# Optimization experiments

Hardware: AMD Instinct MI355X
Metric: run time of the kernel (lower is better)

The kernel has to match this reference:

```python
import jax, jax.numpy as jnp
import numpy as np

B, S, D, H = 2, 2048, 1024, 16
HD = D // H  # head_dim = 64
ROPE_BASE = 10000.0


def _rope_tables(seq_len, head_dim, dtype):
    inv_freq = 1.0 / (ROPE_BASE ** (jnp.arange(0, head_dim, 2, dtype=jnp.float32) / head_dim))
    t = jnp.arange(seq_len, dtype=jnp.float32)
    freqs = jnp.outer(t, inv_freq)                      # [S, HD/2]
    emb = jnp.concatenate([freqs, freqs], axis=-1)      # [S, HD]
    return jnp.cos(emb).astype(dtype), jnp.sin(emb).astype(dtype)


def _rotate_half(x):
    x1, x2 = jnp.split(x, 2, axis=-1)
    return jnp.concatenate([-x2, x1], axis=-1)


def setup_inputs() -> dict:
    key = jax.random.key(0)
    k0, k1, k2, k3, k4 = jax.random.split(key, 5)
    std = 0.02
    return {
        "hidden_states": jax.random.normal(k0, (B, S, D), dtype=jnp.float32),
        "attention_mask": jnp.ones((B, S), dtype=jnp.int32),
        "Wq": jax.random.normal(k1, (D, D), dtype=jnp.float32) * std,
        "Wk": jax.random.normal(k2, (D, D), dtype=jnp.float32) * std,
        "Wv": jax.random.normal(k3, (D, D), dtype=jnp.float32) * std,
        "Wo": jax.random.normal(k4, (D, D), dtype=jnp.float32) * std,
    }


def reference(hidden_states, attention_mask, Wq, Wk, Wv, Wo):
    b, s, d = hidden_states.shape
    scale = HD ** -0.5

    # torch Linear (no bias): y = x @ W.T, then split heads -> [b, h, s, hd]
    def proj_heads(W):
        y = jnp.einsum('bsd,ed->bse', hidden_states, W)
        return y.reshape(b, s, H, HD).transpose(0, 2, 1, 3)

    q, k, v = proj_heads(Wq), proj_heads(Wk), proj_heads(Wv)

    cos, sin = _rope_tables(s, HD, q.dtype)   # [s, hd]
    cos, sin = cos[None, None], sin[None, None]
    q = q * cos + _rotate_half(q) * sin
    k = k * cos + _rotate_half(k) * sin

    attn = jnp.einsum('bhqd,bhkd->bhqk', q, k) * scale  # [b,h,s,s]
    # mask [b,s] broadcast over heads and query dim (matches expand in torch)
    attn = jnp.where(attention_mask[:, None, None, :] == 0, -jnp.inf, attn)
    attn = jax.nn.softmax(attn, axis=-1)

    out = jnp.einsum('bhqk,bhkd->bhqd', attn, v)
    out = out.transpose(0, 2, 1, 3).reshape(b, s, d)
    return jnp.einsum('bsd,ed->bse', out, Wo)
```

## Files before the change

kernel.cpp:

```cpp
#include <hip/hip_runtime.h>
#include <math.h>

#define B_  2
#define S_  2048
#define D_  1024
#define H_  16
#define HD_ 64
#define M_  (B_*S_)

typedef __attribute__((ext_vector_type(8)))  short s8v;
typedef __attribute__((ext_vector_type(4)))  int   i4v;
typedef __attribute__((ext_vector_type(4)))  float f4v;
typedef __attribute__((ext_vector_type(16))) float f16x;
#define MFMA16(a,b,c) __builtin_amdgcn_mfma_f32_16x16x32_bf16(a,b,c,0,0,0)
#define MFMA32(a,b,c) __builtin_amdgcn_mfma_f32_32x32x16_bf16(a,b,c,0,0,0)

typedef __attribute__((address_space(1))) const unsigned int uint_ga;
typedef __attribute__((address_space(3))) unsigned int       uint_ls;

__device__ __forceinline__ unsigned short f2bf(float x) {
    unsigned u = __float_as_uint(x);
    u += 0x7FFF + ((u >> 16) & 1);
    return (unsigned short)(u >> 16);
}
__device__ __forceinline__ void gld16(const unsigned short* g, short* l) {
    __builtin_amdgcn_global_load_lds((uint_ga*)g, (uint_ls*)l, 16, 0, 0);
}

__global__ void rope_table_kernel(float2* __restrict__ cst)
{
    int i = blockIdx.x * 256 + threadIdx.x;
    int j = i >> 11, s = i & 2047;
    double inv = pow(10000.0, -(double)j / 32.0);
    double ang = (double)s * inv;
    cst[i] = make_float2((float)cos(ang), (float)sin(ang));
}

__global__ __launch_bounds__(256) void cvt_bf16_kernel(
    const float* __restrict__ X,  const float* __restrict__ Wq,
    const float* __restrict__ Wk, const float* __restrict__ Wv,
    const float* __restrict__ Wo,
    unsigned short* __restrict__ Xb,  unsigned short* __restrict__ Wqb,
    unsigned short* __restrict__ Wkb, unsigned short* __restrict__ Wvb,
    unsigned short* __restrict__ Wob)
{
    int y = blockIdx.y;
    const float* src = (y==0)?X:(y==1)?Wq:(y==2)?Wk:(y==3)?Wv:Wo;
    unsigned short* dst = (y==0)?Xb:(y==1)?Wqb:(y==2)?Wkb:(y==3)?Wvb:Wob;
    int n = (y==0) ? (M_*D_) : (D_*D_);
    int i = (blockIdx.x*256 + threadIdx.x)*4;
    if (i >= n) return;
    float4 v = *(const float4*)&src[i];
    ushort4 o;
    o.x = f2bf(v.x); o.y = f2bf(v.y); o.z = f2bf(v.z); o.w = f2bf(v.w);
    *(ushort4*)&dst[i] = o;
}

__device__ __forceinline__ void mfma_128x128(
    const unsigned short* __restrict__ Amat, const unsigned short* __restrict__ Bmat,
    int m0, int n0, short* As, short* Bs, f4v acc[4][4])
{
    int tid = threadIdx.x;
    int l = tid & 63, w = tid >> 6;
    int wm = w >> 1, wn = w & 1;
    int lm = l & 15, qd = l >> 4;
    int lm7 = lm & 7;

    f4v z = {0.f, 0.f, 0.f, 0.f};
#pragma unroll
    for (int mt = 0; mt < 4; mt++)
#pragma unroll
        for (int nt = 0; nt < 4; nt++) acc[mt][nt] = z;

    int rl = l >> 3;
    int kc = (l & 7) ^ rl;
    const unsigned short* aG = Amat + (size_t)(m0 + w*32 + rl) * D_ + kc*8;
    const unsigned short* bG = Bmat + (size_t)(n0 + w*32 + rl) * D_ + kc*8;
    short* aL = As + (w*32)*64;
    short* bL = Bs + (w*32)*64;

#pragma unroll 1
    for (int k0 = 0; k0 < D_; k0 += 64) {
        __syncthreads();
#pragma unroll
        for (int j = 0; j < 4; j++) {
            gld16(aG + k0 + (size_t)j*8*D_, aL + j*8*64);
            gld16(bG + k0 + (size_t)j*8*D_, bL + j*8*64);
        }
        __syncthreads();
#pragma unroll
        for (int half = 0; half < 2; half++) {
            int pc = (half*4 + qd) ^ lm7;
            s8v afr[4], bfr[4];
#pragma unroll
            for (int x = 0; x < 4; x++) {
                afr[x] = *(const s8v*)(As + ((wm*64 + x*16 + lm)*8 + pc)*8);
                bfr[x] = *(const s8v*)(Bs + ((wn*64 + x*16 + lm)*8 + pc)*8);
            }
#pragma unroll
            for (int mt = 0; mt < 4; mt++)
#pragma unroll
                for (int nt = 0; nt < 4; nt++)
                    acc[mt][nt] = MFMA16(afr[mt], bfr[nt], acc[mt][nt]);
        }
    }
}

__global__ __launch_bounds__(256, 2) void qkv_mfma_kernel(
    const unsigned short* __restrict__ Xb,
    const unsigned short* __restrict__ Wqb, const unsigned short* __restrict__ Wkb,
    const unsigned short* __restrict__ Wvb, const float2* __restrict__ cst,
    unsigned short* __restrict__ Q, unsigned short* __restrict__ K,
    unsigned short* __restrict__ Vt)
{
    __shared__ __align__(16) short As[8192], Bs[8192];
    int bx = blockIdx.x, by = blockIdx.y;
    int proj = by >> 3, f8 = by & 7;
    int l = threadIdx.x & 63, w = threadIdx.x >> 6;
    int wm = w >> 1, wn = w & 1, lm = l & 15, qd = l >> 4;

    f4v acc[4][4];
    if (proj < 2) {
        const unsigned short* Wm = proj ? Wkb : Wqb;
        mfma_128x128(Wm, Xb, f8*128, bx*128, As, Bs, acc);

        int b  = (bx*128) >> 11;
        int sb = ((bx*128) & 2047) + wn*64;
        int bh = b*H_ + f8*2 + wm;
        unsigned short* dst = proj ? K : Q;
#pragma unroll
        for (int mt = 0; mt < 4; mt++) {
            float sgn = (mt < 2) ? -1.f : 1.f;
#pragma unroll
            for (int nt = 0; nt < 4; nt++) {
                int s = sb + nt*16 + lm;
                unsigned short ov[4];
#pragma unroll
                for (int r = 0; r < 4; r++) {
                    int d = mt*16 + qd*4 + r;
                    float2 cs = cst[(d & 31)*S_ + s];
                    float v = acc[mt][nt][r];
                    float p = acc[mt^2][nt][r];
                    ov[r] = f2bf(v*cs.x + sgn*p*cs.y);
                }
                ushort4 ou; ou.x=ov[0]; ou.y=ov[1]; ou.z=ov[2]; ou.w=ov[3];
                *(ushort4*)&dst[((size_t)bh*S_ + s)*HD_ + mt*16 + qd*4] = ou;
            }
        }
    } else {
        mfma_128x128(Xb, Wvb, bx*128, f8*128, As, Bs, acc);

        int b  = (bx*128) >> 11;
        int sb = ((bx*128) & 2047) + wm*64;
        int bh = b*H_ + f8*2 + wn;
#pragma unroll
        for (int mt = 0; mt < 4; mt++)
#pragma unroll
            for (int nt = 0; nt < 4; nt++) {
                int dim = nt*16 + lm;
                int s   = sb + mt*16 + qd*4;
                ushort4 ou;
                ou.x = f2bf(acc[mt][nt][0]);
                ou.y = f2bf(acc[mt][nt][1]);
                ou.z = f2bf(acc[mt][nt][2]);
                ou.w = f2bf(acc[mt][nt][3]);
                *(ushort4*)&Vt[((size_t)bh*HD_ + dim)*S_ + s] = ou;
            }
    }
}

#define SCALE2 0.1803368801111204f
#define MXF2   16.0f
__global__ __launch_bounds__(256, 2) void flash_mfma_kernel(
    const unsigned short* __restrict__ Q, const unsigned short* __restrict__ K,
    const unsigned short* __restrict__ Vt, const int* __restrict__ mask,
    unsigned short* __restrict__ AO)
{
    __shared__ __align__(16) short Ksh[8192];
    __shared__ __align__(16) short Vsh[8192];
    __shared__ __align__(16) float msk[S_];

    int bh = blockIdx.y;
    int b = bh >> 4, h = bh & 15;
    int tid = threadIdx.x;
    int l = tid & 63, w = tid >> 6;
    int lq = l & 31;
    int hf = l >> 5;
    int q0 = blockIdx.x * 128 + w * 32;

    {
        int i0 = tid * 8;
        const int* mp = mask + b * S_ + i0;
#pragma unroll
        for (int jj = 0; jj < 8; jj++)
            msk[i0 + jj] = mp[jj] ? -MXF2 : -3.0e38f;
    }

    const unsigned short* Qr = Q + ((size_t)bh * S_ + q0 + lq) * HD_ + hf * 8;
    s8v qf[4];
#pragma unroll
    for (int dc = 0; dc < 4; dc++) qf[dc] = *(const s8v*)(Qr + dc * 16);

    f16x zz = {0.f};
    f16x oacc[2]; oacc[0] = zz; oacc[1] = zz;
    float li = 0.f;

    const unsigned short* Kb = K  + (size_t)bh * S_ * HD_;
    const unsigned short* Vb = Vt + (size_t)bh * HD_ * S_;

    int fb0 = 2*w, fb1 = 2*w + 1;
    const unsigned short* kS0 = Kb + (size_t)((fb0>>2)*32 + lq) * HD_ + (fb0&3)*16 + hf*8;
    const unsigned short* kS1 = Kb + (size_t)((fb1>>2)*32 + lq) * HD_ + (fb1&3)*16 + hf*8;
    const unsigned short* vS0 = Vb + (size_t)((fb0>>2)*32 + lq) * S_  + (fb0&3)*16 + hf*8;
    const unsigned short* vS1 = Vb + (size_t)((fb1>>2)*32 + lq) * S_  + (fb1&3)*16 + hf*8;

    s8v kr0 = *(const s8v*)(kS0);
    s8v kr1 = *(const s8v*)(kS1);
    s8v vr0 = *(const s8v*)(vS0);
    s8v vr1 = *(const s8v*)(vS1);

#pragma unroll 1
    for (int t = 0; t < S_ / 64; t++) {
        int buf = (t & 1) * 4096;
        *(s8v*)(Ksh + buf + fb0*512 + l*8) = kr0;
        *(s8v*)(Ksh + buf + fb1*512 + l*8) = kr1;
        *(s8v*)(Vsh + buf + fb0*512 + l*8) = vr0;
        *(s8v*)(Vsh + buf + fb1*512 + l*8) = vr1;
        __syncthreads();
        if (t < S_/64 - 1) {
            int koff = (t + 1) * 64;
            kr0 = *(const s8v*)(kS0 + (size_t)koff * HD_);
            kr1 = *(const s8v*)(kS1 + (size_t)koff * HD_);
            vr0 = *(const s8v*)(vS0 + koff);
            vr1 = *(const s8v*)(vS1 + koff);
        }

        f16x sa0 = zz, sa1 = zz;
#pragma unroll
        for (int dc = 0; dc < 4; dc++) {
            s8v kf0 = *(const s8v*)(Ksh + buf + (0*4 + dc)*512 + l*8);
            sa0 = MFMA32(kf0, qf[dc], sa0);
        }
#pragma unroll
        for (int dc = 0; dc < 4; dc++) {
            s8v kf1 = *(const s8v*)(Ksh + buf + (1*4 + dc)*512 + l*8);
            sa1 = MFMA32(kf1, qf[dc], sa1);
        }

        float p[32];
#pragma unroll
        for (int kt = 0; kt < 2; kt++)
#pragma unroll
            for (int g = 0; g < 4; g++) {
                f4v mv = *(const f4v*)&msk[t*64 + kt*32 + g*8 + hf*4];
#pragma unroll
                for (int i = 0; i < 4; i++) {
                    float raw = (kt == 0) ? sa0[g*4 + i] : sa1[g*4 + i];
                    p[kt*16 + g*4 + i] = exp2f(fmaf(raw, SCALE2, mv[i]));
                }
            }
#pragma unroll
        for (int r = 0; r < 32; r++)
            li += __uint_as_float(__float_as_uint(p[r]) & 0xFFFF0000u);
        int pk[16];
#pragma unroll
        for (int m = 0; m < 16; m++)
            pk[m] = __builtin_amdgcn_perm(__float_as_uint(p[2*m+1]),
                                          __float_as_uint(p[2*m]), 0x07060302);

#pragma unroll
        for (int kc = 0; kc < 4; kc++) {
            int a = 4*kc;
            int x01 = hf ? pk[a]   : pk[a+2];
            int x23 = hf ? pk[a+1] : pk[a+3];
            int y01 = __shfl_xor(x01, 32);
            int y23 = __shfl_xor(x23, 32);
            i4v fr;
            fr.x = hf ? y01 : pk[a];
            fr.y = hf ? y23 : pk[a+1];
            fr.z = hf ? pk[a+2] : y01;
            fr.w = hf ? pk[a+3] : y23;
            s8v pf = __builtin_bit_cast(s8v, fr);
#pragma unroll
            for (int dt = 0; dt < 2; dt++) {
                s8v vf = *(const s8v*)(Vsh + buf + (dt*4 + kc)*512 + l*8);
                oacc[dt] = MFMA32(vf, pf, oacc[dt]);
            }
        }
        __syncthreads();
    }

    li += __shfl_xor(li, 32);
    float invl = 1.0f / li;
    int qtok = q0 + lq;
    unsigned short* Or = AO + ((size_t)(b * S_ + qtok)) * D_ + h * HD_;
#pragma unroll
    for (int dt = 0; dt < 2; dt++)
#pragma unroll
        for (int g = 0; g < 4; g++) {
            int d0 = dt*32 + g*8 + hf*4;
            ushort4 o;
            o.x = f2bf(oacc[dt][g*4 + 0] * invl);
            o.y = f2bf(oacc[dt][g*4 + 1] * invl);
            o.z = f2bf(oacc[dt][g*4 + 2] * invl);
            o.w = f2bf(oacc[dt][g*4 + 3] * invl);
            *(ushort4*)&Or[d0] = o;
        }
}

__global__ __launch_bounds__(256, 2) void outproj_mfma_kernel(
    const unsigned short* __restrict__ AO, const unsigned short* __restrict__ Wob,
    float* __restrict__ out)
{
    __shared__ __align__(16) short As[8192], Bs[8192];
    int bx = blockIdx.x, by = blockIdx.y;
    int l = threadIdx.x & 63, w = threadIdx.x >> 6;
    int wm = w >> 1, wn = w & 1, lm = l & 15, qd = l >> 4;

    f4v acc[4][4];
    mfma_128x128(Wob, AO, by*128, bx*128, As, Bs, acc);

#pragma unroll
    for (int mt = 0; mt < 4; mt++)
#pragma unroll
        for (int nt = 0; nt < 4; nt++) {
            int tok = bx*128 + wn*64 + nt*16 + lm;
            int e   = by*128 + wm*64 + mt*16 + qd*4;
            *(f4v*)&out[(size_t)tok*D_ + e] = acc[mt][nt];
        }
}

extern "C" void kernel_launch(void* const* d_in, const int* in_sizes, int n_in,
                              void* d_out, int out_size, void* d_ws, size_t ws_size,
                              hipStream_t stream)
{
    const float* X    = (const float*)d_in[0];
    const int*   mask = (const int*)  d_in[1];
    const float* Wq   = (const float*)d_in[2];
    const float* Wk   = (const float*)d_in[3];
    const float* Wv   = (const float*)d_in[4];
    const float* Wo   = (const float*)d_in[5];
    float* out = (float*)d_out;

    unsigned short* ws = (unsigned short*)d_ws;
    unsigned short* Xb  = ws;
    unsigned short* Wqb = Xb  + (size_t)M_ * D_;
    unsigned short* Wkb = Wqb + (size_t)D_ * D_;
    unsigned short* Wvb = Wkb + (size_t)D_ * D_;
    unsigned short* Wob = Wvb + (size_t)D_ * D_;
    unsigned short* Qb  = Wob + (size_t)D_ * D_;
    unsigned short* Kb  = Qb  + (size_t)M_ * D_;
    unsigned short* Vtb = Kb  + (size_t)M_ * D_;
    unsigned short* AOb = Vtb + (size_t)M_ * D_;
    float2* cst = (float2*)(AOb + (size_t)M_ * D_);

    rope_table_kernel<<<(S_ * 32) / 256, 256, 0, stream>>>(cst);
    cvt_bf16_kernel<<<dim3(4096, 5), 256, 0, stream>>>(
        X, Wq, Wk, Wv, Wo, Xb, Wqb, Wkb, Wvb, Wob);
    qkv_mfma_kernel<<<dim3(32, 24), 256, 0, stream>>>(
        Xb, Wqb, Wkb, Wvb, cst, Qb, Kb, Vtb);
    flash_mfma_kernel<<<dim3(S_ / 128, B_ * H_), 256, 0, stream>>>(
        Qb, Kb, Vtb, mask, AOb);
    outproj_mfma_kernel<<<dim3(32, 8), 256, 0, stream>>>(AOb, Wob, out);
}
```

Before: 209.4 us.

## Async LDS loads in flash loop, MFMA row sums, fold scale into Q, merge rope kernel

The flash kernel now loads K/V tiles directly into LDS with global_load_lds and double buffers them, which drops the register staging and one barrier per iteration. The softmax denominator is computed by an extra MFMA against a vector of ones instead of 32 scalar adds per lane. The softmax scale is folded into Q during the QKV epilogue, which removes an FMA per score. The rope table computation is merged into the conversion kernel to save one launch. The risks are bf16 rounding of the pre-scaled Q and a possible race, since the next-buffer async load is issued while other waves may still be reading the previous buffer; the trailing barrier appears to protect against this.

```diff
diff --git a/kernel.cpp b/kernel.cpp
--- a/kernel.cpp
+++ b/kernel.cpp
@@ -27,14 +27,8 @@
     __builtin_amdgcn_global_load_lds((uint_ga*)g, (uint_ls*)l, 16, 0, 0);
 }
 
-__global__ void rope_table_kernel(float2* __restrict__ cst)
-{
-    int i = blockIdx.x * 256 + threadIdx.x;
-    int j = i >> 11, s = i & 2047;
-    double inv = pow(10000.0, -(double)j / 32.0);
-    double ang = (double)s * inv;
-    cst[i] = make_float2((float)cos(ang), (float)sin(ang));
-}
+#define SCALE2 0.1803368801111204f
+#define MXF2   16.0f
 
 __global__ __launch_bounds__(256) void cvt_bf16_kernel(
     const float* __restrict__ X,  const float* __restrict__ Wq,
@@ -42,9 +36,19 @@
     const float* __restrict__ Wo,
     unsigned short* __restrict__ Xb,  unsigned short* __restrict__ Wqb,
     unsigned short* __restrict__ Wkb, unsigned short* __restrict__ Wvb,
-    unsigned short* __restrict__ Wob)
+    unsigned short* __restrict__ Wob, float2* __restrict__ cst)
 {
     int y = blockIdx.y;
+    if (y == 5) {
+        int i = blockIdx.x * 256 + threadIdx.x;
+        if (i < S_ * 32) {
+            int j = i >> 11, s = i & 2047;
+            double inv = pow(10000.0, -(double)j / 32.0);
+            double ang = (double)s * inv;
+            cst[i] = make_float2((float)cos(ang), (float)sin(ang));
+        }
+        return;
+    }
     const float* src = (y==0)?X:(y==1)?Wq:(y==2)?Wk:(y==3)?Wv:Wo;
     unsigned short* dst = (y==0)?Xb:(y==1)?Wqb:(y==2)?Wkb:(y==3)?Wvb:Wob;
     int n = (y==0) ? (M_*D_) : (D_*D_);
@@ -128,6 +132,7 @@
         int sb = ((bx*128) & 2047) + wn*64;
         int bh = b*H_ + f8*2 + wm;
         unsigned short* dst = proj ? K : Q;
+        float post = proj ? 1.0f : SCALE2;
 #pragma unroll
         for (int mt = 0; mt < 4; mt++) {
             float sgn = (mt < 2) ? -1.f : 1.f;
@@ -141,7 +146,7 @@
                     float2 cs = cst[(d & 31)*S_ + s];
                     float v = acc[mt][nt][r];
                     float p = acc[mt^2][nt][r];
-                    ov[r] = f2bf(v*cs.x + sgn*p*cs.y);
+                    ov[r] = f2bf((v*cs.x + sgn*p*cs.y) * post);
                 }
                 ushort4 ou; ou.x=ov[0]; ou.y=ov[1]; ou.z=ov[2]; ou.w=ov[3];
                 *(ushort4*)&dst[((size_t)bh*S_ + s)*HD_ + mt*16 + qd*4] = ou;
@@ -169,8 +174,6 @@
     }
 }
 
-#define SCALE2 0.1803368801111204f
-#define MXF2   16.0f
 __global__ __launch_bounds__(256, 2) void flash_mfma_kernel(
     const unsigned short* __restrict__ Q, const unsigned short* __restrict__ K,
     const unsigned short* __restrict__ Vt, const int* __restrict__ mask,
@@ -203,7 +206,10 @@
 
     f16x zz = {0.f};
     f16x oacc[2]; oacc[0] = zz; oacc[1] = zz;
-    float li = 0.f;
+    f16x lacc = zz;
+    s8v ones;
+#pragma unroll
+    for (int j = 0; j < 8; j++) ones[j] = (short)0x3F80;
 
     const unsigned short* Kb = K  + (size_t)bh * S_ * HD_;
     const unsigned short* Vb = Vt + (size_t)bh * HD_ * S_;
@@ -214,25 +220,22 @@
     const unsigned short* vS0 = Vb + (size_t)((fb0>>2)*32 + lq) * S_  + (fb0&3)*16 + hf*8;
     const unsigned short* vS1 = Vb + (size_t)((fb1>>2)*32 + lq) * S_  + (fb1&3)*16 + hf*8;
 
-    s8v kr0 = *(const s8v*)(kS0);
-    s8v kr1 = *(const s8v*)(kS1);
-    s8v vr0 = *(const s8v*)(vS0);
-    s8v vr1 = *(const s8v*)(vS1);
+    gld16(kS0, Ksh + fb0*512);
+    gld16(kS1, Ksh + fb1*512);
+    gld16(vS0, Vsh + fb0*512);
+    gld16(vS1, Vsh + fb1*512);
+    __syncthreads();
 
 #pragma unroll 1
     for (int t = 0; t < S_ / 64; t++) {
-        int buf = (t & 1) * 4096;
-        *(s8v*)(Ksh + buf + fb0*512 + l*8) = kr0;
-        *(s8v*)(Ksh + buf + fb1*512 + l*8) = kr1;
-        *(s8v*)(Vsh + buf + fb0*512 + l*8) = vr0;
-        *(s8v*)(Vsh + buf + fb1*512 + l*8) = vr1;
-        __syncthreads();
+        int buf  = (t & 1) * 4096;
+        int nbuf = 4096 - buf;
         if (t < S_/64 - 1) {
             int koff = (t + 1) * 64;
-            kr0 = *(const s8v*)(kS0 + (size_t)koff * HD_);
-            kr1 = *(const s8v*)(kS1 + (size_t)koff * HD_);
-            vr0 = *(const s8v*)(vS0 + koff);
-            vr1 = *(const s8v*)(vS1 + koff);
+            gld16(kS0 + (size_t)koff * HD_, Ksh + nbuf + fb0*512);
+            gld16(kS1 + (size_t)koff * HD_, Ksh + nbuf + fb1*512);
+            gld16(vS0 + koff,               Vsh + nbuf + fb0*512);
+            gld16(vS1 + koff,               Vsh + nbuf + fb1*512);
         }
 
         f16x sa0 = zz, sa1 = zz;
@@ -256,12 +259,9 @@
 #pragma unroll
                 for (int i = 0; i < 4; i++) {
                     float raw = (kt == 0) ? sa0[g*4 + i] : sa1[g*4 + i];
-                    p[kt*16 + g*4 + i] = exp2f(fmaf(raw, SCALE2, mv[i]));
+                    p[kt*16 + g*4 + i] = exp2f(raw + mv[i]);
                 }
             }
-#pragma unroll
-        for (int r = 0; r < 32; r++)
-            li += __uint_as_float(__float_as_uint(p[r]) & 0xFFFF0000u);
         int pk[16];
 #pragma unroll
         for (int m = 0; m < 16; m++)
@@ -269,8 +269,8 @@
                                           __float_as_uint(p[2*m]), 0x07060302);
 
 #pragma unroll
-        for (int kc = 0; kc < 4; kc++) {
-            int a = 4*kc;
+        for (int kcc = 0; kcc < 4; kcc++) {
+            int a = 4*kcc;
             int x01 = hf ? pk[a]   : pk[a+2];
             int x23 = hf ? pk[a+1] : pk[a+3];
             int y01 = __shfl_xor(x01, 32);
@@ -283,15 +283,15 @@
             s8v pf = __builtin_bit_cast(s8v, fr);
 #pragma unroll
             for (int dt = 0; dt < 2; dt++) {
-                s8v vf = *(const s8v*)(Vsh + buf + (dt*4 + kc)*512 + l*8);
+                s8v vf = *(const s8v*)(Vsh + buf + (dt*4 + kcc)*512 + l*8);
                 oacc[dt] = MFMA32(vf, pf, oacc[dt]);
             }
+            lacc = MFMA32(ones, pf, lacc);
         }
         __syncthreads();
     }
 
-    li += __shfl_xor(li, 32);
-    float invl = 1.0f / li;
+    float invl = 1.0f / lacc[0];
     int qtok = q0 + lq;
     unsigned short* Or = AO + ((size_t)(b * S_ + qtok)) * D_ + h * HD_;
 #pragma unroll
@@ -354,9 +354,8 @@
     unsigned short* AOb = Vtb + (size_t)M_ * D_;
     float2* cst = (float2*)(AOb + (size_t)M_ * D_);
 
-    rope_table_kernel<<<(S_ * 32) / 256, 256, 0, stream>>>(cst);
-    cvt_bf16_kernel<<<dim3(4096, 5), 256, 0, stream>>>(
-        X, Wq, Wk, Wv, Wo, Xb, Wqb, Wkb, Wvb, Wob);
+    cvt_bf16_kernel<<<dim3(4096, 6), 256, 0, stream>>>(
+        X, Wq, Wk, Wv, Wo, Xb, Wqb, Wkb, Wvb, Wob, cst);
     qkv_mfma_kernel<<<dim3(32, 24), 256, 0, stream>>>(
         Xb, Wqb, Wkb, Wvb, cst, Qb, Kb, Vtb);
     flash_mfma_kernel<<<dim3(S_ / 128, B_ * H_), 256, 0, stream>>>(
```

Result: no change. 208.5 us (-0.4%).
